# Optimization experiments

Hardware: AMD Instinct MI355X
Metric: run time of the kernel (lower is better)

Reference implementation:

```python
import jax, jax.numpy as jnp
import numpy as np

B, N, D, S, H = 32, 4096, 256, 16, 512
ITERS = 3
EPS = 1e-8
LN_EPS = 1e-5  # torch LayerNorm default


def _ln(x, w, b):
    m = jnp.mean(x, axis=-1, keepdims=True)
    v = jnp.mean(jnp.square(x - m), axis=-1, keepdims=True)
    return (x - m) / jnp.sqrt(v + LN_EPS) * w + b


def setup_inputs() -> dict:
    key = jax.random.key(0)
    ks = jax.random.split(key, 20)
    s = 1.0 / np.sqrt(D)
    return {
        "inputs": jax.random.normal(ks[0], (B, N, D), jnp.float32),
        "token_weight": jax.random.uniform(ks[1], (B, N), jnp.float32),
        "noise": jax.random.normal(ks[2], (B, S, D), jnp.float32),
        "ln_in_w": jnp.ones((D,), jnp.float32), "ln_in_b": jnp.zeros((D,), jnp.float32),
        "ln_s_w": jnp.ones((D,), jnp.float32), "ln_s_b": jnp.zeros((D,), jnp.float32),
        "ln_m_w": jnp.ones((D,), jnp.float32), "ln_m_b": jnp.zeros((D,), jnp.float32),
        "Wk": jax.random.normal(ks[3], (D, D), jnp.float32) * s,
        "Wv": jax.random.normal(ks[4], (D, D), jnp.float32) * s,
        "Wq": jax.random.normal(ks[5], (D, D), jnp.float32) * s,
        "gru_wih": jax.random.normal(ks[6], (3 * D, D), jnp.float32) * s,
        "gru_whh": jax.random.normal(ks[7], (3 * D, D), jnp.float32) * s,
        "gru_bih": jax.random.normal(ks[8], (3 * D,), jnp.float32) * s,
        "gru_bhh": jax.random.normal(ks[9], (3 * D,), jnp.float32) * s,
        "mlp_w1": jax.random.normal(ks[10], (H, D), jnp.float32) * s,
        "mlp_b1": jnp.zeros((H,), jnp.float32),
        "mlp_w2": jax.random.normal(ks[11], (D, H), jnp.float32) * (1.0 / np.sqrt(H)),
        "mlp_b2": jnp.zeros((D,), jnp.float32),
        "slots_mu": jax.random.normal(ks[12], (1, 1, D), jnp.float32) * 0.02,
        "slots_logsigma": jax.random.normal(ks[13], (1, 1, D), jnp.float32) * 0.02,
    }


def _gru(x, h, wih, whh, bih, bhh):
    # torch GRUCell: gates ordered r, z, n
    gi = x @ wih.T + bih  # [BS, 3D]
    gh = h @ whh.T + bhh
    ir, iz, inn = jnp.split(gi, 3, axis=-1)
    hr, hz, hn = jnp.split(gh, 3, axis=-1)
    r = jax.nn.sigmoid(ir + hr)
    z = jax.nn.sigmoid(iz + hz)
    n = jnp.tanh(inn + r * hn)
    return (1.0 - z) * n + z * h


def reference(inputs, token_weight, noise, ln_in_w, ln_in_b, ln_s_w, ln_s_b,
              ln_m_w, ln_m_b, Wk, Wv, Wq, gru_wih, gru_whh, gru_bih, gru_bhh,
              mlp_w1, mlp_b1, mlp_w2, mlp_b2, slots_mu, slots_logsigma):
    tw = jnp.clip(token_weight, 0.0, None)  # [B,N]
    x = _ln(inputs, ln_in_w, ln_in_b)
    k = x @ Wk.T  # [B,N,D]
    v = x @ Wv.T
    sigma = jnp.clip(jnp.exp(slots_logsigma), 1e-6, None)
    slots = slots_mu + sigma * noise  # [B,S,D]
    scale = D ** (-0.5)
    attn = None
    for _ in range(ITERS):
        slots_prev = slots
        q = _ln(slots, ln_s_w, ln_s_b) @ Wq.T  # [B,S,D]
        logits = jnp.einsum('bnd,bmd->bnm', k, q) * scale  # [B,N,S]
        attn = jax.nn.softmax(logits, axis=-1)  # softmax over slots
        attn = attn * tw[:, :, None]
        attn = attn / (jnp.sum(attn, axis=1, keepdims=True) + EPS)  # normalize over tokens
        updates = jnp.einsum('bnm,bnd->bmd', attn, v)  # [B,S,D]
        slots = _gru(updates.reshape(B * S, D), slots_prev.reshape(B * S, D),
                     gru_wih, gru_whh, gru_bih, gru_bhh).reshape(B, S, D)
        h = jax.nn.gelu(_ln(slots, ln_m_w, ln_m_b) @ mlp_w1.T + mlp_b1, approximate=False)
        slots = slots + h @ mlp_w2.T + mlp_b2
    return slots, attn
```

## Files before the change

### kernel.cpp

```cpp
#include <hip/hip_runtime.h>
#include <hip/hip_bf16.h>
#include <math.h>


#define EPS_ 1e-8f
#define LNEPS_ 1e-5f
#define XSW(r) ((((r)&7)<<3) ^ ((((r)>>3)&3)<<4))

typedef __attribute__((ext_vector_type(8))) short bf16x8;
typedef __attribute__((ext_vector_type(4))) float f32x4;
typedef __attribute__((ext_vector_type(4))) short s16x4;

static __device__ __forceinline__ short f2bf(float f) {
  __hip_bfloat16 h = __float2bfloat16(f);
  union { __hip_bfloat16 h; short s; } u; u.h = h; return u.s;
}
static __device__ __forceinline__ float4 ld4(const float* p){ return *(const float4*)p; }

__global__ __launch_bounds__(256) void k_prep(
    const float* __restrict__ Wq, const float* __restrict__ Wk,
    const float* __restrict__ wih, const float* __restrict__ Wv,
    const float* __restrict__ whh, const float* __restrict__ w1, const float* __restrict__ w2,
    short* __restrict__ MTb, short* __restrict__ Mb, short* __restrict__ whhb,
    short* __restrict__ w1b, short* __restrict__ w2b) {
  int blk = blockIdx.x, t = threadIdx.x;
  if (blk < 64) {
    int e0 = blk*4;
    float a0=0,a1=0,a2=0,a3=0;
    for (int d=0; d<256; d++) {
      float qv = Wq[d*256 + t];
      a0 += qv*Wk[d*256+e0];   a1 += qv*Wk[d*256+e0+1];
      a2 += qv*Wk[d*256+e0+2]; a3 += qv*Wk[d*256+e0+3];
    }
    MTb[(e0  )*256+t]=f2bf(a0); MTb[(e0+1)*256+t]=f2bf(a1);
    MTb[(e0+2)*256+t]=f2bf(a2); MTb[(e0+3)*256+t]=f2bf(a3);
  } else if (blk < 256) {
    int n0 = (blk-64)*4;
    float a0=0,a1=0,a2=0,a3=0;
    for (int d=0; d<256; d++) {
      float vv = Wv[d*256 + t];
      a0 += wih[(n0  )*256+d]*vv; a1 += wih[(n0+1)*256+d]*vv;
      a2 += wih[(n0+2)*256+d]*vv; a3 += wih[(n0+3)*256+d]*vv;
    }
    Mb[(size_t)(n0  )*256+t]=f2bf(a0); Mb[(size_t)(n0+1)*256+t]=f2bf(a1);
    Mb[(size_t)(n0+2)*256+t]=f2bf(a2); Mb[(size_t)(n0+3)*256+t]=f2bf(a3);
  } else {
    int c = (blk-256)*256 + t;
    const float* src; short* dst;
    if (c < 49152) { src=whh; dst=whhb; }
    else if ((c-=49152) < 32768) { src=w1; dst=w1b; }
    else { c-=32768; src=w2; dst=w2b; }
    float4 v = ld4(src + (size_t)c*4);
    short4 o; o.x=f2bf(v.x); o.y=f2bf(v.y); o.z=f2bf(v.z); o.w=f2bf(v.w);
    *(short4*)(dst + (size_t)c*4) = o;
  }
}

template<int LNIN, int WATTN>
__global__ __launch_bounds__(256) void k3(
    const float* __restrict__ inputs, const float* __restrict__ lnw, const float* __restrict__ lnb,
    short* __restrict__ xbf, const short* __restrict__ qk, const float* __restrict__ twg,
    float* __restrict__ ux_part, float* __restrict__ colsum_part, float* __restrict__ attn_un) {
  __shared__ __align__(16) short Xs[64*256];
  __shared__ __align__(16) short Pt[16*72];
  __shared__ float tws[64];
  __shared__ float cs[16];
  __shared__ float lnwb[512];
  const int t = threadIdx.x;
  const int b = blockIdx.x >> 4;
  const int n0 = (blockIdx.x & 15) * 256;
  const int lane = t & 63, w = t >> 6, l15 = lane & 15, lg = lane >> 4;
  bf16x8 qkf[8];
  {
    const short* qrow = qk + ((size_t)(b*16+l15))*256 + lg*8;
    #pragma unroll
    for (int kk=0;kk<8;kk++) qkf[kk] = *(const bf16x8*)(qrow + kk*32);
  }
  if (LNIN){
    if (t < 64)       *(float4*)&lnwb[t*4]           = ld4(lnw + t*4);
    else if (t < 128) *(float4*)&lnwb[256+(t-64)*4]  = ld4(lnb + (t-64)*4);
  }
  if (t<16) cs[t]=0.f;
  f32x4 uacc[4] = {};
  const int srow = t>>5, sck = t&31;
  uint4 pf[8];
  if (!LNIN){
    const short* xg = xbf + ((size_t)b*4096 + n0)*256;
    #pragma unroll
    for (int r8=0;r8<8;r8++)
      pf[r8] = *(const uint4*)&xg[(size_t)(r8*8+srow)*256 + sck*8];
  }
  for (int g=0; g<4; ++g) {
    __syncthreads();
    const size_t rowbase = (size_t)b*4096 + n0 + g*64;
    if (LNIN) {
      const float* ing = inputs + rowbase*256;
      const int r = t>>2, c = t&3;
      float4 vv[16];
      #pragma unroll
      for (int k=0;k<16;k++) vv[k] = ld4(ing + r*256 + (c+4*k)*4);
      float s=0.f, sq=0.f;
      #pragma unroll
      for (int k=0;k<16;k++){
        s  += vv[k].x+vv[k].y+vv[k].z+vv[k].w;
        sq += vv[k].x*vv[k].x+vv[k].y*vv[k].y+vv[k].z*vv[k].z+vv[k].w*vv[k].w;
      }
      s += __shfl_xor(s,1);  s += __shfl_xor(s,2);
      sq += __shfl_xor(sq,1); sq += __shfl_xor(sq,2);
      float mean = s*(1.f/256.f);
      float rstd = rsqrtf(sq*(1.f/256.f) - mean*mean + LNEPS_);
      short* xw = xbf + rowbase*256;
      const int sw = XSW(r);
      #pragma unroll
      for (int k=0;k<16;k++){
        int d0 = (c+4*k)*4;
        float4 wv = *(float4*)&lnwb[d0];
        float4 bv = *(float4*)&lnwb[256+d0];
        s16x4 pk;
        pk[0]=f2bf((vv[k].x-mean)*rstd*wv.x+bv.x);
        pk[1]=f2bf((vv[k].y-mean)*rstd*wv.y+bv.y);
        pk[2]=f2bf((vv[k].z-mean)*rstd*wv.z+bv.z);
        pk[3]=f2bf((vv[k].w-mean)*rstd*wv.w+bv.w);
        *(s16x4*)&Xs[r*256 + (d0 ^ sw)] = pk;
        *(s16x4*)&xw[r*256 + d0] = pk;
      }
    } else {
      #pragma unroll
      for (int r8=0;r8<8;r8++){
        int row = r8*8+srow;
        *(uint4*)&Xs[row*256 + ((sck*8) ^ XSW(row))] = pf[r8];
      }
    }
    if (t<64) tws[t] = fmaxf(twg[rowbase + t], 0.f);
    __syncthreads();
    if (!LNIN && g<3){
      const short* xg = xbf + (rowbase+64)*256;
      #pragma unroll
      for (int r8=0;r8<8;r8++)
        pf[r8] = *(const uint4*)&xg[(size_t)(r8*8+srow)*256 + sck*8];
    }
    f32x4 acc = {0.f,0.f,0.f,0.f};
    {
      const int ra = w*16+l15, sa = XSW(ra);
      #pragma unroll
      for (int kk=0;kk<8;kk++){
        bf16x8 af = *(const bf16x8*)&Xs[ra*256 + ((kk*32+lg*8) ^ sa)];
        acc = __builtin_amdgcn_mfma_f32_16x16x32_bf16(af, qkf[kk], acc, 0,0,0);
      }
    }
    float a4[4];
    #pragma unroll
    for (int q=0;q<4;q++){
      float v = acc[q]*0.0625f;
      float m = v;
      #pragma unroll
      for (int d=1; d<16; d<<=1) m = fmaxf(m, __shfl_xor(m, d, 16));
      float e = __expf(v-m);
      float se = e;
      #pragma unroll
      for (int d=1; d<16; d<<=1) se += __shfl_xor(se, d, 16);
      int row = w*16 + lg*4 + q;
      float a = (e/se)*tws[row];
      a4[q] = a;
      if (WATTN)
        attn_un[(rowbase + row)*16 + l15] = a;
    }
    float psum = a4[0]+a4[1]+a4[2]+a4[3];
    psum += __shfl_xor(psum, 16);
    psum += __shfl_xor(psum, 32);
    if (lane<16) atomicAdd(&cs[l15], psum);
    s16x4 pk; pk[0]=f2bf(a4[0]); pk[1]=f2bf(a4[1]); pk[2]=f2bf(a4[2]); pk[3]=f2bf(a4[3]);
    *(s16x4*)&Pt[l15*72 + w*16 + lg*4] = pk;
    __syncthreads();
    #pragma unroll
    for (int kk=0;kk<2;kk++){
      bf16x8 a2 = *(const bf16x8*)&Pt[l15*72 + kk*32 + lg*8];
      #pragma unroll
      for (int tt=0;tt<4;tt++){
        int col = w*64 + tt*16 + l15;
        bf16x8 b2;
        #pragma unroll
        for (int j=0;j<8;j++){
          int r2 = kk*32 + lg*8 + j;
          b2[j] = Xs[r2*256 + (col ^ XSW(r2))];
        }
        uacc[tt] = __builtin_amdgcn_mfma_f32_16x16x32_bf16(a2, b2, uacc[tt], 0,0,0);
      }
    }
  }
  __syncthreads();
  if (t<16) colsum_part[blockIdx.x*16 + t] = cs[t];
  #pragma unroll
  for (int tt=0;tt<4;tt++){
    #pragma unroll
    for (int q=0;q<4;q++)
      ux_part[(size_t)blockIdx.x*4096 + (lg*4+q)*256 + w*64 + tt*16 + l15] = uacc[tt][q];
  }
}

__global__ __launch_bounds__(256) void k_reduce(const float* __restrict__ uxp,
    const float* __restrict__ csp, short* __restrict__ uxr, float* __restrict__ csr) {
  int r = blockIdx.x;
  int b = r>>4, s = r&15;
  int t = threadIdx.x;
  float cs = 0.f;
  #pragma unroll
  for (int k=0;k<16;k++) cs += csp[((b<<4)+k)*16 + s];
  float u = 0.f;
  #pragma unroll
  for (int k=0;k<16;k++) u += uxp[(size_t)((b<<4)+k)*4096 + s*256 + t];
  uxr[(size_t)r*256+t] = f2bf(u/(cs+EPS_));
  if (t==0) csr[r] = cs;
}

__global__ __launch_bounds__(256) void k_gigh(
    const short* __restrict__ uxr, const short* __restrict__ slotsb,
    const short* __restrict__ Mb, const short* __restrict__ whhb,
    const float* __restrict__ bih, const float* __restrict__ bhh,
    float* __restrict__ gig) {
  __shared__ short As[64*40];
  __shared__ short Ws[64*40];
  const int t=threadIdx.x, bn=blockIdx.x, bm=blockIdx.y;
  const short* A; const short* W; const float* bias; int wo;
  if (bn<12) { A=uxr;    W=Mb   + (size_t)bn*64*256;      bias=bih; wo=bn*64; }
  else       { A=slotsb; W=whhb + (size_t)(bn-12)*64*256; bias=bhh; wo=(bn-12)*64; }
  const int w=t>>6, lane=t&63, l15=lane&15, lg=lane>>4;
  f32x4 acc[4]={};
  for (int k0=0;k0<256;k0+=32){
    __syncthreads();
    *(uint4*)&As[(t>>2)*40+(t&3)*8] = *(const uint4*)&A[(size_t)(bm*64+(t>>2))*256 + k0 + (t&3)*8];
    *(uint4*)&Ws[(t>>2)*40+(t&3)*8] = *(const uint4*)&W[(size_t)(t>>2)*256 + k0 + (t&3)*8];
    __syncthreads();
    bf16x8 af = *(const bf16x8*)&As[(w*16+l15)*40+lg*8];
    #pragma unroll
    for (int ct=0;ct<4;ct++){
      bf16x8 bfr = *(const bf16x8*)&Ws[(ct*16+l15)*40+lg*8];
      acc[ct]=__builtin_amdgcn_mfma_f32_16x16x32_bf16(af,bfr,acc[ct],0,0,0);
    }
  }
  #pragma unroll
  for (int ct=0;ct<4;ct++){
    float bv = bias[wo + ct*16 + l15];
    #pragma unroll
    for (int q=0;q<4;q++){
      int row = bm*64 + w*16 + lg*4 + q;
      gig[(size_t)row*1536 + bn*64 + ct*16 + l15] = acc[ct][q] + bv;
    }
  }
}

__global__ __launch_bounds__(256) void k_mlp1(
    const short* __restrict__ lnmb, const short* __restrict__ w1b,
    const float* __restrict__ b1, short* __restrict__ hb) {
  __shared__ short As[64*40];
  __shared__ short Ws[64*40];
  const int t=threadIdx.x, bn=blockIdx.x, bm=blockIdx.y;
  const int w=t>>6, lane=t&63, l15=lane&15, lg=lane>>4;
  f32x4 acc[4]={};
  for (int k0=0;k0<256;k0+=32){
    __syncthreads();
    *(uint4*)&As[(t>>2)*40+(t&3)*8] = *(const uint4*)&lnmb[(size_t)(bm*64+(t>>2))*256 + k0 + (t&3)*8];
    *(uint4*)&Ws[(t>>2)*40+(t&3)*8] = *(const uint4*)&w1b[(size_t)(bn*64+(t>>2))*256 + k0 + (t&3)*8];
    __syncthreads();
    bf16x8 af = *(const bf16x8*)&As[(w*16+l15)*40+lg*8];
    #pragma unroll
    for (int ct=0;ct<4;ct++){
      bf16x8 bfr = *(const bf16x8*)&Ws[(ct*16+l15)*40+lg*8];
      acc[ct]=__builtin_amdgcn_mfma_f32_16x16x32_bf16(af,bfr,acc[ct],0,0,0);
    }
  }
  #pragma unroll
  for (int ct=0;ct<4;ct++){
    float bv = b1[bn*64 + ct*16 + l15];
    #pragma unroll
    for (int q=0;q<4;q++){
      int row = bm*64 + w*16 + lg*4 + q;
      float v = acc[ct][q] + bv;
      v = 0.5f*v*(1.f+erff(v*0.70710678118654752f));
      hb[(size_t)row*512 + bn*64 + ct*16 + l15] = f2bf(v);
    }
  }
}

__global__ __launch_bounds__(256) void k_gates(const float* __restrict__ gig,
    const float* __restrict__ lw, const float* __restrict__ lb,
    float* __restrict__ slots, short* __restrict__ lnmb) {
  int row  = blockIdx.x*4 + (threadIdx.x>>6);
  int lane = threadIdx.x & 63;
  const float* gi = gig + (size_t)row*1536 + lane*4;
  float4 ir = ld4(gi), iz = ld4(gi+256), inn = ld4(gi+512);
  float4 hr = ld4(gi+768), hz = ld4(gi+1024), hn = ld4(gi+1280);
  float* sp = slots + (size_t)row*256 + lane*4;
  float4 h = ld4(sp);
  float hp[4];
  {
    float r0 = 1.f/(1.f+__expf(-(ir.x+hr.x))); float z0 = 1.f/(1.f+__expf(-(iz.x+hz.x)));
    hp[0] = (1.f-z0)*tanhf(inn.x + r0*hn.x) + z0*h.x;
    float r1 = 1.f/(1.f+__expf(-(ir.y+hr.y))); float z1 = 1.f/(1.f+__expf(-(iz.y+hz.y)));
    hp[1] = (1.f-z1)*tanhf(inn.y + r1*hn.y) + z1*h.y;
    float r2 = 1.f/(1.f+__expf(-(ir.z+hr.z))); float z2 = 1.f/(1.f+__expf(-(iz.z+hz.z)));
    hp[2] = (1.f-z2)*tanhf(inn.z + r2*hn.z) + z2*h.z;
    float r3 = 1.f/(1.f+__expf(-(ir.w+hr.w))); float z3 = 1.f/(1.f+__expf(-(iz.w+hz.w)));
    hp[3] = (1.f-z3)*tanhf(inn.w + r3*hn.w) + z3*h.w;
  }
  float s = hp[0]+hp[1]+hp[2]+hp[3];
  float sq = hp[0]*hp[0]+hp[1]*hp[1]+hp[2]*hp[2]+hp[3]*hp[3];
  #pragma unroll
  for (int d=1; d<64; d<<=1) { s += __shfl_xor(s,d); sq += __shfl_xor(sq,d); }
  float mean = s*(1.f/256.f);
  float rstd = rsqrtf(sq*(1.f/256.f) - mean*mean + LNEPS_);
  float4 wv = ld4(lw+lane*4), bv = ld4(lb+lane*4);
  *(float4*)sp = make_float4(hp[0],hp[1],hp[2],hp[3]);
  short4 o;
  o.x = f2bf((hp[0]-mean)*rstd*wv.x+bv.x);
  o.y = f2bf((hp[1]-mean)*rstd*wv.y+bv.y);
  o.z = f2bf((hp[2]-mean)*rstd*wv.z+bv.z);
  o.w = f2bf((hp[3]-mean)*rstd*wv.w+bv.w);
  *(short4*)(lnmb + (size_t)row*256 + lane*4) = o;
}

template<int MODE>
__global__ __launch_bounds__(256) void k_slotend(
    const short* __restrict__ hb, const short* __restrict__ w2b, const float* __restrict__ b2,
    const float* __restrict__ mu, const float* __restrict__ ls, const float* __restrict__ noise,
    const float* __restrict__ res, float* __restrict__ sout, short* __restrict__ slotsb,
    const float* __restrict__ lnsw, const float* __restrict__ lnsb,
    const short* __restrict__ MTb, short* __restrict__ qk) {
  __shared__ short As[64*40];
  __shared__ short Ws[256*40];
  __shared__ short lnS[64*264];
  const int t=threadIdx.x, bm=blockIdx.x;
  const int w=t>>6, lane=t&63, l15=lane&15, lg=lane>>4;
  float v[16][4];
  if (MODE==1) {
    #pragma unroll
    for (int ct=0;ct<16;ct++){
      int col = ct*16+l15;
      float m = mu[col], sg = fmaxf(__expf(ls[col]),1e-6f);
      #pragma unroll
      for (int q=0;q<4;q++){
        int row = bm*64 + w*16 + lg*4 + q;
        v[ct][q] = m + sg*noise[(size_t)row*256+col];
      }
    }
  } else {
    f32x4 acc[16]={};
    for (int k0=0;k0<512;k0+=32){
      __syncthreads();
      *(uint4*)&As[(t>>2)*40+(t&3)*8] = *(const uint4*)&hb[(size_t)(bm*64+(t>>2))*512 + k0 + (t&3)*8];
      #pragma unroll
      for (int i=0;i<4;i++){ int idx=t+i*256;
        *(uint4*)&Ws[(idx>>2)*40+(idx&3)*8] = *(const uint4*)&w2b[(size_t)(idx>>2)*512 + k0 + (idx&3)*8]; }
      __syncthreads();
      bf16x8 af = *(const bf16x8*)&As[(w*16+l15)*40+lg*8];
      #pragma unroll
      for (int ct=0;ct<16;ct++){
        bf16x8 bfr = *(const bf16x8*)&Ws[(ct*16+l15)*40+lg*8];
        acc[ct]=__builtin_amdgcn_mfma_f32_16x16x32_bf16(af,bfr,acc[ct],0,0,0);
      }
    }
    #pragma unroll
    for (int ct=0;ct<16;ct++){
      int col = ct*16+l15;
      float bv = b2[col];
      #pragma unroll
      for (int q=0;q<4;q++){
        int row = bm*64 + w*16 + lg*4 + q;
        v[ct][q] = acc[ct][q] + bv + res[(size_t)row*256+col];
      }
    }
  }
  float s[4]={0,0,0,0}, sq[4]={0,0,0,0};
  #pragma unroll
  for (int ct=0;ct<16;ct++)
    #pragma unroll
    for (int q=0;q<4;q++){ s[q]+=v[ct][q]; sq[q]+=v[ct][q]*v[ct][q]; }
  #pragma unroll
  for (int q=0;q<4;q++){
    #pragma unroll
    for (int d=1; d<16; d<<=1){ s[q]+=__shfl_xor(s[q],d,16); sq[q]+=__shfl_xor(sq[q],d,16); }
  }
  #pragma unroll
  for (int ct=0;ct<16;ct++){
    int col = ct*16+l15;
    float lw = (MODE!=2) ? lnsw[col] : 0.f;
    float lb = (MODE!=2) ? lnsb[col] : 0.f;
    #pragma unroll
    for (int q=0;q<4;q++){
      int row = bm*64 + w*16 + lg*4 + q;
      sout[(size_t)row*256+col] = v[ct][q];
      if (MODE!=2){
        float mean = s[q]*(1.f/256.f);
        float rstd = rsqrtf(sq[q]*(1.f/256.f)-mean*mean+LNEPS_);
        slotsb[(size_t)row*256+col] = f2bf(v[ct][q]);
        lnS[(w*16+lg*4+q)*264 + col] = f2bf((v[ct][q]-mean)*rstd*lw+lb);
      }
    }
  }
  if (MODE!=2){
    f32x4 qa[16]={};
    for (int k0=0;k0<256;k0+=32){
      __syncthreads();
      #pragma unroll
      for (int i=0;i<4;i++){ int idx=t+i*256;
        *(uint4*)&Ws[(idx>>2)*40+(idx&3)*8] = *(const uint4*)&MTb[(size_t)(idx>>2)*256 + k0 + (idx&3)*8]; }
      __syncthreads();
      bf16x8 af = *(const bf16x8*)&lnS[(w*16+l15)*264 + k0 + lg*8];
      #pragma unroll
      for (int ct=0;ct<16;ct++){
        bf16x8 bfr = *(const bf16x8*)&Ws[(ct*16+l15)*40+lg*8];
        qa[ct]=__builtin_amdgcn_mfma_f32_16x16x32_bf16(af,bfr,qa[ct],0,0,0);
      }
    }
    #pragma unroll
    for (int ct=0;ct<16;ct++)
      #pragma unroll
      for (int q=0;q<4;q++)
        qk[(size_t)(bm*64+w*16+lg*4+q)*256 + ct*16+l15] = f2bf(qa[ct][q]);
  }
}

__global__ __launch_bounds__(256) void k_attn_norm(float* __restrict__ au,
    const float* __restrict__ cs) {
  size_t i = ((size_t)blockIdx.x*256 + threadIdx.x)*4;
  float4 v = ld4(au + i);
  int s = (int)(i & 15);
  size_t b = i >> 16;
  const float* c = cs + b*16 + s;
  float4 o;
  o.x = v.x/(c[0]+EPS_); o.y = v.y/(c[1]+EPS_);
  o.z = v.z/(c[2]+EPS_); o.w = v.w/(c[3]+EPS_);
  *(float4*)(au + i) = o;
}

extern "C" void kernel_launch(void* const* d_in, const int* in_sizes, int n_in,
                              void* d_out, int out_size, void* d_ws, size_t ws_size,
                              hipStream_t stream) {
  const float* inputs   = (const float*)d_in[0];
  const float* token_w  = (const float*)d_in[1];
  const float* noise    = (const float*)d_in[2];
  const float* ln_in_w  = (const float*)d_in[3];
  const float* ln_in_b  = (const float*)d_in[4];
  const float* ln_s_w   = (const float*)d_in[5];
  const float* ln_s_b   = (const float*)d_in[6];
  const float* ln_m_w   = (const float*)d_in[7];
  const float* ln_m_b   = (const float*)d_in[8];
  const float* Wk       = (const float*)d_in[9];
  const float* Wv       = (const float*)d_in[10];
  const float* Wq       = (const float*)d_in[11];
  const float* gru_wih  = (const float*)d_in[12];
  const float* gru_whh  = (const float*)d_in[13];
  const float* gru_bih  = (const float*)d_in[14];
  const float* gru_bhh  = (const float*)d_in[15];
  const float* mlp_w1   = (const float*)d_in[16];
  const float* mlp_b1   = (const float*)d_in[17];
  const float* mlp_w2   = (const float*)d_in[18];
  const float* mlp_b2   = (const float*)d_in[19];
  const float* slots_mu = (const float*)d_in[20];
  const float* slots_ls = (const float*)d_in[21];

  float* out_slots = (float*)d_out;
  float* out_attn  = out_slots + 131072;

  char* wsb = (char*)d_ws;
  size_t off = 0;
  short* xbf     = (short*)(wsb + off); off += 67108864;
  float* ux_part = (float*)(wsb + off); off += 8388608;
  float* cs_part = (float*)(wsb + off); off += 32768;
  float* cs_red  = (float*)(wsb + off); off += 2048;
  short* qk      = (short*)(wsb + off); off += 262144;
  short* uxr     = (short*)(wsb + off); off += 262144;
  short* MTb     = (short*)(wsb + off); off += 131072;
  short* Mb      = (short*)(wsb + off); off += 393216;
  float* gig     = (float*)(wsb + off); off += 3145728;
  float* slots   = (float*)(wsb + off); off += 524288;
  short* slotsb  = (short*)(wsb + off); off += 262144;
  short* lnmb    = (short*)(wsb + off); off += 262144;
  short* hb      = (short*)(wsb + off); off += 524288;
  short* whhb    = (short*)(wsb + off); off += 393216;
  short* w1b     = (short*)(wsb + off); off += 262144;
  short* w2b     = (short*)(wsb + off); off += 262144;

  k_prep<<<704,256,0,stream>>>(Wq, Wk, gru_wih, Wv, gru_whh, mlp_w1, mlp_w2,
                               MTb, Mb, whhb, w1b, w2b);
  k_slotend<1><<<8,256,0,stream>>>(nullptr, nullptr, nullptr, slots_mu, slots_ls, noise,
                                   nullptr, slots, slotsb, ln_s_w, ln_s_b, MTb, qk);
  for (int it=0; it<3; ++it) {
    if (it==0)
      k3<1,0><<<512,256,0,stream>>>(inputs, ln_in_w, ln_in_b, xbf, qk, token_w,
                                    ux_part, cs_part, out_attn);
    else if (it==1)
      k3<0,0><<<512,256,0,stream>>>(inputs, ln_in_w, ln_in_b, xbf, qk, token_w,
                                    ux_part, cs_part, out_attn);
    else
      k3<0,1><<<512,256,0,stream>>>(inputs, ln_in_w, ln_in_b, xbf, qk, token_w,
                                    ux_part, cs_part, out_attn);
    k_reduce<<<512,256,0,stream>>>(ux_part, cs_part, uxr, cs_red);
    k_gigh<<<dim3(24,8),256,0,stream>>>(uxr, slotsb, Mb, whhb, gru_bih, gru_bhh, gig);
    k_gates<<<128,256,0,stream>>>(gig, ln_m_w, ln_m_b, slots, lnmb);
    k_mlp1<<<dim3(8,8),256,0,stream>>>(lnmb, w1b, mlp_b1, hb);
    if (it<2)
      k_slotend<0><<<8,256,0,stream>>>(hb, w2b, mlp_b2, nullptr, nullptr, nullptr,
                                       slots, slots, slotsb, ln_s_w, ln_s_b, MTb, qk);
    else
      k_slotend<2><<<8,256,0,stream>>>(hb, w2b, mlp_b2, nullptr, nullptr, nullptr,
                                       slots, out_slots, slotsb, ln_s_w, ln_s_b, MTb, qk);
  }
  k_attn_norm<<<2048,256,0,stream>>>(out_attn, cs_red);
}
```

Before: 273.8 us.

## Make k3 wave-independent with per-wave LDS tiles and bf16 partials

The attention/update kernel k3 now has each wave own a 32-row LDS tile and process 64 tokens on its own, so the block-wide __syncthreads and shared colsum atomics go away. Each wave keeps all 16 output column tiles in registers and writes its own bf16 partial, so k_reduce now sums 64 partials per batch instead of 16. The LN-input path writes normalized x back to global from LDS in coalesced form, and launch bounds request two blocks per CU. In exchange it uses more registers, writes four times as many partials, and rounds partial sums to bf16, which may cost accuracy.

After: 537.3 us. 96.2% more time.

```diff
diff --git a/kernel.cpp b/kernel.cpp
--- a/kernel.cpp
+++ b/kernel.cpp
@@ -14,6 +14,9 @@
 static __device__ __forceinline__ short f2bf(float f) {
   __hip_bfloat16 h = __float2bfloat16(f);
   union { __hip_bfloat16 h; short s; } u; u.h = h; return u.s;
+}
+static __device__ __forceinline__ float bf2f(short s) {
+  union { float f; unsigned u; } x; x.u = ((unsigned)(unsigned short)s) << 16; return x.f;
 }
 static __device__ __forceinline__ float4 ld4(const float* p){ return *(const float4*)p; }
 
@@ -57,158 +60,168 @@
 }
 
 template<int LNIN, int WATTN>
-__global__ __launch_bounds__(256) void k3(
+__global__ __launch_bounds__(256, 2) void k3(
     const float* __restrict__ inputs, const float* __restrict__ lnw, const float* __restrict__ lnb,
     short* __restrict__ xbf, const short* __restrict__ qk, const float* __restrict__ twg,
-    float* __restrict__ ux_part, float* __restrict__ colsum_part, float* __restrict__ attn_un) {
-  __shared__ __align__(16) short Xs[64*256];
-  __shared__ __align__(16) short Pt[16*72];
-  __shared__ float tws[64];
-  __shared__ float cs[16];
-  __shared__ float lnwb[512];
-  const int t = threadIdx.x;
+    short* __restrict__ ux_part, float* __restrict__ colsum_part, float* __restrict__ attn_un) {
+  __shared__ __align__(16) short XsAll[4][32*256];
+  __shared__ __align__(16) short PtAll[4][16*40];
+  const int lane = threadIdx.x & 63, w = threadIdx.x >> 6;
+  const int l15 = lane & 15, lg = lane >> 4;
   const int b = blockIdx.x >> 4;
-  const int n0 = (blockIdx.x & 15) * 256;
-  const int lane = t & 63, w = t >> 6, l15 = lane & 15, lg = lane >> 4;
+  const size_t wrow0 = (size_t)b*4096 + (blockIdx.x & 15)*256 + w*64;
+  short* xs = &XsAll[w][0];
+  short* pt = &PtAll[w][0];
   bf16x8 qkf[8];
   {
     const short* qrow = qk + ((size_t)(b*16+l15))*256 + lg*8;
     #pragma unroll
     for (int kk=0;kk<8;kk++) qkf[kk] = *(const bf16x8*)(qrow + kk*32);
   }
-  if (LNIN){
-    if (t < 64)       *(float4*)&lnwb[t*4]           = ld4(lnw + t*4);
-    else if (t < 128) *(float4*)&lnwb[256+(t-64)*4]  = ld4(lnb + (t-64)*4);
-  }
-  if (t<16) cs[t]=0.f;
-  f32x4 uacc[4] = {};
-  const int srow = t>>5, sck = t&31;
-  uint4 pf[8];
+  f32x4 acc[16] = {};
+  float cs_acc = 0.f;
+  uint4 pf[16];
   if (!LNIN){
-    const short* xg = xbf + ((size_t)b*4096 + n0)*256;
-    #pragma unroll
-    for (int r8=0;r8<8;r8++)
-      pf[r8] = *(const uint4*)&xg[(size_t)(r8*8+srow)*256 + sck*8];
-  }
-  for (int g=0; g<4; ++g) {
-    __syncthreads();
-    const size_t rowbase = (size_t)b*4096 + n0 + g*64;
-    if (LNIN) {
-      const float* ing = inputs + rowbase*256;
-      const int r = t>>2, c = t&3;
-      float4 vv[16];
-      #pragma unroll
-      for (int k=0;k<16;k++) vv[k] = ld4(ing + r*256 + (c+4*k)*4);
-      float s=0.f, sq=0.f;
-      #pragma unroll
-      for (int k=0;k<16;k++){
-        s  += vv[k].x+vv[k].y+vv[k].z+vv[k].w;
-        sq += vv[k].x*vv[k].x+vv[k].y*vv[k].y+vv[k].z*vv[k].z+vv[k].w*vv[k].w;
-      }
-      s += __shfl_xor(s,1);  s += __shfl_xor(s,2);
-      sq += __shfl_xor(sq,1); sq += __shfl_xor(sq,2);
-      float mean = s*(1.f/256.f);
-      float rstd = rsqrtf(sq*(1.f/256.f) - mean*mean + LNEPS_);
-      short* xw = xbf + rowbase*256;
-      const int sw = XSW(r);
-      #pragma unroll
-      for (int k=0;k<16;k++){
-        int d0 = (c+4*k)*4;
-        float4 wv = *(float4*)&lnwb[d0];
-        float4 bv = *(float4*)&lnwb[256+d0];
-        s16x4 pk;
-        pk[0]=f2bf((vv[k].x-mean)*rstd*wv.x+bv.x);
-        pk[1]=f2bf((vv[k].y-mean)*rstd*wv.y+bv.y);
-        pk[2]=f2bf((vv[k].z-mean)*rstd*wv.z+bv.z);
-        pk[3]=f2bf((vv[k].w-mean)*rstd*wv.w+bv.w);
-        *(s16x4*)&Xs[r*256 + (d0 ^ sw)] = pk;
-        *(s16x4*)&xw[r*256 + d0] = pk;
+    const short* xg = xbf + wrow0*256;
+    #pragma unroll
+    for (int i=0;i<16;i++){
+      int row = ((i>>3)<<4) + l15;
+      pf[i] = *(const uint4*)&xg[(size_t)row*256 + (i&7)*32 + lg*8];
+    }
+  }
+  for (int tl=0; tl<2; ++tl){
+    const size_t rowb = wrow0 + tl*32;
+    if (LNIN){
+      #pragma unroll
+      for (int sub=0; sub<2; ++sub){
+        const int r32 = sub*16 + l15;
+        const float* ing = inputs + (rowb + r32)*256 + lg*64;
+        float4 vv[16];
+        #pragma unroll
+        for (int k=0;k<16;k++) vv[k] = ld4(ing + k*4);
+        float s=0.f, sq=0.f;
+        #pragma unroll
+        for (int k=0;k<16;k++){
+          s  += vv[k].x+vv[k].y+vv[k].z+vv[k].w;
+          sq += vv[k].x*vv[k].x+vv[k].y*vv[k].y+vv[k].z*vv[k].z+vv[k].w*vv[k].w;
+        }
+        s += __shfl_xor(s,16);  s += __shfl_xor(s,32);
+        sq += __shfl_xor(sq,16); sq += __shfl_xor(sq,32);
+        float mean = s*(1.f/256.f);
+        float rstd = rsqrtf(sq*(1.f/256.f) - mean*mean + LNEPS_);
+        const int sw = XSW(r32);
+        #pragma unroll
+        for (int k=0;k<16;k++){
+          int d0 = lg*64 + k*4;
+          float4 wv = ld4(lnw + d0);
+          float4 bv = ld4(lnb + d0);
+          s16x4 pk;
+          pk[0]=f2bf((vv[k].x-mean)*rstd*wv.x+bv.x);
+          pk[1]=f2bf((vv[k].y-mean)*rstd*wv.y+bv.y);
+          pk[2]=f2bf((vv[k].z-mean)*rstd*wv.z+bv.z);
+          pk[3]=f2bf((vv[k].w-mean)*rstd*wv.w+bv.w);
+          *(s16x4*)&xs[r32*256 + (d0 ^ sw)] = pk;
+        }
       }
     } else {
       #pragma unroll
-      for (int r8=0;r8<8;r8++){
-        int row = r8*8+srow;
-        *(uint4*)&Xs[row*256 + ((sck*8) ^ XSW(row))] = pf[r8];
-      }
-    }
-    if (t<64) tws[t] = fmaxf(twg[rowbase + t], 0.f);
-    __syncthreads();
-    if (!LNIN && g<3){
-      const short* xg = xbf + (rowbase+64)*256;
-      #pragma unroll
-      for (int r8=0;r8<8;r8++)
-        pf[r8] = *(const uint4*)&xg[(size_t)(r8*8+srow)*256 + sck*8];
-    }
-    f32x4 acc = {0.f,0.f,0.f,0.f};
+      for (int i=0;i<16;i++){
+        int r32 = ((i>>3)<<4) + l15;
+        *(uint4*)&xs[r32*256 + ((((i&7)*32) + lg*8) ^ XSW(r32))] = pf[i];
+      }
+      if (tl==0){
+        const short* xg = xbf + (wrow0+32)*256;
+        #pragma unroll
+        for (int i=0;i<16;i++){
+          int row = ((i>>3)<<4) + l15;
+          pf[i] = *(const uint4*)&xg[(size_t)row*256 + (i&7)*32 + lg*8];
+        }
+      }
+    }
+    #pragma unroll
+    for (int sub=0; sub<2; ++sub){
+      const int ra = sub*16 + l15, sa = XSW(ra);
+      f32x4 a1 = {0.f,0.f,0.f,0.f};
+      #pragma unroll
+      for (int kk=0;kk<8;kk++){
+        bf16x8 af = *(const bf16x8*)&xs[ra*256 + ((kk*32+lg*8) ^ sa)];
+        a1 = __builtin_amdgcn_mfma_f32_16x16x32_bf16(af, qkf[kk], a1, 0,0,0);
+      }
+      float a4[4];
+      #pragma unroll
+      for (int q=0;q<4;q++){
+        float v = a1[q]*0.0625f;
+        float m = v;
+        #pragma unroll
+        for (int d=1; d<16; d<<=1) m = fmaxf(m, __shfl_xor(m, d, 16));
+        float e = __expf(v-m);
+        float se = e;
+        #pragma unroll
+        for (int d=1; d<16; d<<=1) se += __shfl_xor(se, d, 16);
+        int rloc = sub*16 + lg*4 + q;
+        float tw = fmaxf(twg[rowb + rloc], 0.f);
+        float a = (e/se)*tw;
+        a4[q] = a;
+        if (WATTN)
+          attn_un[(rowb + rloc)*16 + l15] = a;
+      }
+      float psum = a4[0]+a4[1]+a4[2]+a4[3];
+      psum += __shfl_xor(psum, 16);
+      psum += __shfl_xor(psum, 32);
+      cs_acc += psum;
+      s16x4 pk; pk[0]=f2bf(a4[0]); pk[1]=f2bf(a4[1]); pk[2]=f2bf(a4[2]); pk[3]=f2bf(a4[3]);
+      *(s16x4*)&pt[l15*40 + sub*16 + lg*4] = pk;
+    }
     {
-      const int ra = w*16+l15, sa = XSW(ra);
-      #pragma unroll
-      for (int kk=0;kk<8;kk++){
-        bf16x8 af = *(const bf16x8*)&Xs[ra*256 + ((kk*32+lg*8) ^ sa)];
-        acc = __builtin_amdgcn_mfma_f32_16x16x32_bf16(af, qkf[kk], acc, 0,0,0);
-      }
-    }
-    float a4[4];
-    #pragma unroll
-    for (int q=0;q<4;q++){
-      float v = acc[q]*0.0625f;
-      float m = v;
-      #pragma unroll
-      for (int d=1; d<16; d<<=1) m = fmaxf(m, __shfl_xor(m, d, 16));
-      float e = __expf(v-m);
-      float se = e;
-      #pragma unroll
-      for (int d=1; d<16; d<<=1) se += __shfl_xor(se, d, 16);
-      int row = w*16 + lg*4 + q;
-      float a = (e/se)*tws[row];
-      a4[q] = a;
-      if (WATTN)
-        attn_un[(rowbase + row)*16 + l15] = a;
-    }
-    float psum = a4[0]+a4[1]+a4[2]+a4[3];
-    psum += __shfl_xor(psum, 16);
-    psum += __shfl_xor(psum, 32);
-    if (lane<16) atomicAdd(&cs[l15], psum);
-    s16x4 pk; pk[0]=f2bf(a4[0]); pk[1]=f2bf(a4[1]); pk[2]=f2bf(a4[2]); pk[3]=f2bf(a4[3]);
-    *(s16x4*)&Pt[l15*72 + w*16 + lg*4] = pk;
-    __syncthreads();
-    #pragma unroll
-    for (int kk=0;kk<2;kk++){
-      bf16x8 a2 = *(const bf16x8*)&Pt[l15*72 + kk*32 + lg*8];
-      #pragma unroll
-      for (int tt=0;tt<4;tt++){
-        int col = w*64 + tt*16 + l15;
+      bf16x8 pa = *(const bf16x8*)&pt[l15*40 + lg*8];
+      #pragma unroll
+      for (int et=0; et<16; ++et){
         bf16x8 b2;
         #pragma unroll
         for (int j=0;j<8;j++){
-          int r2 = kk*32 + lg*8 + j;
-          b2[j] = Xs[r2*256 + (col ^ XSW(r2))];
+          int r2 = lg*8 + j;
+          b2[j] = xs[r2*256 + ((et*16+l15) ^ XSW(r2))];
         }
-        uacc[tt] = __builtin_amdgcn_mfma_f32_16x16x32_bf16(a2, b2, uacc[tt], 0,0,0);
-      }
-    }
-  }
-  __syncthreads();
-  if (t<16) colsum_part[blockIdx.x*16 + t] = cs[t];
-  #pragma unroll
-  for (int tt=0;tt<4;tt++){
+        acc[et] = __builtin_amdgcn_mfma_f32_16x16x32_bf16(pa, b2, acc[et], 0,0,0);
+      }
+    }
+    if (LNIN){
+      short* xg = xbf + rowb*256;
+      #pragma unroll
+      for (int i=0;i<16;i++){
+        int idx = lane + i*64;
+        int r32 = idx>>5, ck = idx&31;
+        uint4 vq = *(const uint4*)&xs[r32*256 + ((ck*8) ^ XSW(r32))];
+        *(uint4*)&xg[(size_t)r32*256 + ck*8] = vq;
+      }
+    }
+  }
+  const int wgid = blockIdx.x*4 + w;
+  if (lane < 16) colsum_part[wgid*16 + lane] = cs_acc;
+  #pragma unroll
+  for (int et=0;et<16;et++)
     #pragma unroll
     for (int q=0;q<4;q++)
-      ux_part[(size_t)blockIdx.x*4096 + (lg*4+q)*256 + w*64 + tt*16 + l15] = uacc[tt][q];
-  }
-}
-
-__global__ __launch_bounds__(256) void k_reduce(const float* __restrict__ uxp,
+      xs[(lg*4+q)*256 + et*16 + l15] = f2bf(acc[et][q]);
+  short* up = ux_part + (size_t)wgid*4096;
+  #pragma unroll
+  for (int i=0;i<8;i++){
+    int idx = lane + i*64;
+    *(uint4*)&up[idx*8] = *(const uint4*)&xs[idx*8];
+  }
+}
+
+__global__ __launch_bounds__(256) void k_reduce(const short* __restrict__ uxp,
     const float* __restrict__ csp, short* __restrict__ uxr, float* __restrict__ csr) {
   int r = blockIdx.x;
   int b = r>>4, s = r&15;
   int t = threadIdx.x;
   float cs = 0.f;
-  #pragma unroll
-  for (int k=0;k<16;k++) cs += csp[((b<<4)+k)*16 + s];
+  #pragma unroll 8
+  for (int k=0;k<64;k++) cs += csp[((b<<6)+k)*16 + s];
   float u = 0.f;
-  #pragma unroll
-  for (int k=0;k<16;k++) u += uxp[(size_t)((b<<4)+k)*4096 + s*256 + t];
+  #pragma unroll 8
+  for (int k=0;k<64;k++) u += bf2f(uxp[(size_t)((b<<6)+k)*4096 + s*256 + t]);
   uxr[(size_t)r*256+t] = f2bf(u/(cs+EPS_));
   if (t==0) csr[r] = cs;
 }
@@ -465,8 +478,8 @@
   char* wsb = (char*)d_ws;
   size_t off = 0;
   short* xbf     = (short*)(wsb + off); off += 67108864;
-  float* ux_part = (float*)(wsb + off); off += 8388608;
-  float* cs_part = (float*)(wsb + off); off += 32768;
+  short* ux_part = (short*)(wsb + off); off += 16777216;
+  float* cs_part = (float*)(wsb + off); off += 131072;
   float* cs_red  = (float*)(wsb + off); off += 2048;
   short* qk      = (short*)(wsb + off); off += 262144;
   short* uxr     = (short*)(wsb + off); off += 262144;
```
